# Optimization experiments

Hardware: AMD Instinct MI355X
Metric: run time of the kernel (lower is better)

Reference implementation:

```python
import jax, jax.numpy as jnp
import numpy as np

# init config (must satisfy k1+...+k6 == N_HEAD; k1==0 makes the source's
# off-by-k1 slice indices in get_sinusoid coincide with the correct ones)
K1, K2, K3, K4, K5, K6 = 0, 2, 2, 2, 1, 1
N_HEAD = K1 + K2 + K3 + K4 + K5 + K6  # 8
DILATIONS = (2.0, 4.0, 8.0, 16.0)     # length k4+k5+k6
TRUNC = 200.0                          # hard-coded T[T > 200] = 0 threshold


def setup_inputs() -> dict:
    key = jax.random.key(0)
    k_eta, k_nu, k_theta = jax.random.split(key, 3)
    return {
        "eta": jax.random.uniform(k_eta, (1, 1, 1), dtype=jnp.float32),  # >0 so tanh(eta)>0
        "nu": jax.random.normal(k_nu, (1, 1, 1), dtype=jnp.float32),
        "theta": jax.random.normal(k_theta, (1, 1, 1), dtype=jnp.float32),
        "query_len": 2048,
        "key_len": 2048,
    }


def reference(eta, nu, theta, query_len, key_len):
    k1, k2, k3, k4, k5, k6 = K1, K2, K3, K4, K5, K6
    undil_n = k1 + k2 + k3

    # --- Toeplitz |i-j| matrix, truncated: entries > 200 zeroed ---
    i = jnp.arange(query_len, dtype=jnp.float32)[:, None]
    j = jnp.arange(key_len, dtype=jnp.float32)[None, :]
    T = jnp.abs(i - j)                       # (Lq, Lk)
    T = jnp.where(T > TRUNC, 0.0, T)

    # --- dilated heads: L/d where L % d == 0 else 0 (vectorized over heads) ---
    d = jnp.asarray(DILATIONS, dtype=jnp.float32)[:, None, None]  # (dil_n,1,1)
    ind = (jnp.mod(T[None], d) == 0).astype(jnp.float32)
    Ld = (T[None] / d) * ind                 # (dil_n, Lq, Lk)

    Lu = jnp.broadcast_to(T[None], (undil_n, query_len, key_len))
    L = jnp.concatenate([Lu, Ld], axis=0)    # (n_head, Lq, Lk)

    lambda_ = jnp.tanh(eta)
    gamma = jax.nn.sigmoid(nu)

    # --- sinusoids (slice indices replicate the source exactly; k1=0) ---
    M = L * theta
    s2 = jnp.cos(M[k1:k1 + k2])
    s3 = jnp.sin(M[k2:k2 + k3])
    s5 = jnp.cos(M[k2 + k3 + k4:k2 + k3 + k4 + k5])
    s6 = jnp.sin(M[k2 + k3 + k4 + k5:])

    L1 = L[:k1]
    L2 = L[k1:k1 + k2]
    L3 = L[k1 + k2:k1 + k2 + k3]
    L4 = L[k1 + k2 + k3:k1 + k2 + k3 + k4]
    L5 = L[k1 + k2 + k3 + k4:k1 + k2 + k3 + k4 + k5]
    L6 = L[k1 + k2 + k3 + k4 + k5:]

    P1 = jnp.power(lambda_, L1)
    P4 = jnp.power(lambda_, L4)
    P2 = jnp.power(gamma, L2) * s2
    P3 = jnp.power(gamma, L3) * s3
    P5 = jnp.power(gamma, L5) * s5
    P6 = jnp.power(gamma, L6) * s6

    REM = jnp.concatenate([P1, P2, P3, P4, P5, P6], axis=0)  # (n_head, Lq, Lk)
    return jnp.transpose(REM, (1, 2, 0))                      # (Lq, Lk, n_head)
```

## Files before the change

kernel.cpp:

```cpp
#include <hip/hip_runtime.h>


#define EXP2F(x) __builtin_amdgcn_exp2f(x)
#define LOG2F(x) __builtin_amdgcn_logf(x)
#define SIN_RAD(x) __builtin_amdgcn_sinf((x) * 0.15915494309189535f)
#define COS_RAD(x) __builtin_amdgcn_cosf((x) * 0.15915494309189535f)

__global__ __launch_bounds__(256) void rem_kernel(
    const float* __restrict__ eta_p,
    const float* __restrict__ nu_p,
    const float* __restrict__ theta_p,
    const int*   __restrict__ klen_p,
    float* __restrict__ out,
    int total)
{
    int idx = blockIdx.x * 256 + threadIdx.x;
    if (idx >= total) return;

    int kl = klen_p[0];
    int i  = idx / kl;
    int j  = idx - i * kl;
    int d  = i - j;
    int Ti = d < 0 ? -d : d;
    if (Ti > 200) Ti = 0;

    float eta   = eta_p[0];
    float nu    = nu_p[0];
    float theta = theta_p[0];
    float e2e = EXP2F(2.0f * eta * 1.4426950408889634f);
    float lam = (e2e - 1.0f) / (e2e + 1.0f);
    float gam = 1.0f / (1.0f + EXP2F(-nu * 1.4426950408889634f));
    float l2l = LOG2F(lam);
    float l2g = LOG2F(gam);

    float Tf = (float)Ti;
    float c = COS_RAD(theta * Tf);
    float s = SIN_RAD(theta * Tf);
    float gT = EXP2F(Tf * l2g);
    float v01 = gT * c;
    float v23 = gT * s;

    float L2f  = (Ti & 1)  ? 0.0f : (float)(Ti >> 1);
    float L4f  = (Ti & 3)  ? 0.0f : (float)(Ti >> 2);
    float L8f  = (Ti & 7)  ? 0.0f : (float)(Ti >> 3);
    float L16f = (Ti & 15) ? 0.0f : (float)(Ti >> 4);

    float v4 = EXP2F(L2f * l2l);
    float v5 = EXP2F(L4f * l2l);
    float v6 = EXP2F(L8f  * l2g) * COS_RAD(theta * L8f);
    float v7 = EXP2F(L16f * l2g) * SIN_RAD(theta * L16f);

    float4* o = (float4*)(out + (size_t)idx * 8);
    o[0] = make_float4(v01, v01, v23, v23);
    o[1] = make_float4(v4, v5, v6, v7);
}

extern "C" void kernel_launch(void* const* d_in, const int* in_sizes, int n_in,
                              void* d_out, int out_size, void* d_ws, size_t ws_size,
                              hipStream_t stream) {
    const float* eta   = (const float*)d_in[0];
    const float* nu    = (const float*)d_in[1];
    const float* theta = (const float*)d_in[2];
    const int* klen = (const int*)d_in[4];

    int total = out_size / 8;
    int blocks = (total + 255) / 256;
    rem_kernel<<<blocks, 256, 0, stream>>>(eta, nu, theta, klen,
                                           (float*)d_out, total);
}
```

Baseline: 143.0 us.

## Split per-pair work across threads, fast-path truncated zeros, precompute scalars

```diff
diff --git a/kernel.cpp b/kernel.cpp
--- a/kernel.cpp
+++ b/kernel.cpp
@@ -3,56 +3,68 @@
 
 #define EXP2F(x) __builtin_amdgcn_exp2f(x)
 #define LOG2F(x) __builtin_amdgcn_logf(x)
-#define SIN_RAD(x) __builtin_amdgcn_sinf((x) * 0.15915494309189535f)
-#define COS_RAD(x) __builtin_amdgcn_cosf((x) * 0.15915494309189535f)
+#define SINR(x)  __builtin_amdgcn_sinf(x)
+#define COSR(x)  __builtin_amdgcn_cosf(x)
+#define INV2PI 0.15915494309189535f
+#define LOG2E  1.4426950408889634f
 
-__global__ __launch_bounds__(256) void rem_kernel(
-    const float* __restrict__ eta_p,
-    const float* __restrict__ nu_p,
-    const float* __restrict__ theta_p,
+__global__ void rem_setup(const float* __restrict__ eta,
+                          const float* __restrict__ nu,
+                          const float* __restrict__ theta,
+                          float* __restrict__ ws)
+{
+    if (threadIdx.x == 0 && blockIdx.x == 0) {
+        float e2e = EXP2F(2.0f * eta[0] * LOG2E);
+        float lam = (e2e - 1.0f) / (e2e + 1.0f);
+        float gam = 1.0f / (1.0f + EXP2F(-nu[0] * LOG2E));
+        ws[0] = LOG2F(lam);
+        ws[1] = LOG2F(gam);
+        ws[2] = theta[0] * INV2PI;
+    }
+}
+
+__global__ __launch_bounds__(256) void rem_main(
+    const float* __restrict__ ws,
     const int*   __restrict__ klen_p,
     float* __restrict__ out,
-    int total)
+    int nquads)
 {
-    int idx = blockIdx.x * 256 + threadIdx.x;
-    if (idx >= total) return;
+    int q = blockIdx.x * 256 + threadIdx.x;
+    if (q >= nquads) return;
 
-    int kl = klen_p[0];
-    int i  = idx / kl;
-    int j  = idx - i * kl;
-    int d  = i - j;
-    int Ti = d < 0 ? -d : d;
+    int kl   = klen_p[0];
+    int pair = q >> 1;
+    int sel  = q & 1;
+    int i    = pair / kl;
+    int j    = pair - i * kl;
+    int d    = i - j;
+    int Ti   = d < 0 ? -d : d;
     if (Ti > 200) Ti = 0;
 
-    float eta   = eta_p[0];
-    float nu    = nu_p[0];
-    float theta = theta_p[0];
-    float e2e = EXP2F(2.0f * eta * 1.4426950408889634f);
-    float lam = (e2e - 1.0f) / (e2e + 1.0f);
-    float gam = 1.0f / (1.0f + EXP2F(-nu * 1.4426950408889634f));
-    float l2l = LOG2F(lam);
-    float l2g = LOG2F(gam);
-
-    float Tf = (float)Ti;
-    float c = COS_RAD(theta * Tf);
-    float s = SIN_RAD(theta * Tf);
-    float gT = EXP2F(Tf * l2g);
-    float v01 = gT * c;
-    float v23 = gT * s;
-
-    float L2f  = (Ti & 1)  ? 0.0f : (float)(Ti >> 1);
-    float L4f  = (Ti & 3)  ? 0.0f : (float)(Ti >> 2);
-    float L8f  = (Ti & 7)  ? 0.0f : (float)(Ti >> 3);
-    float L16f = (Ti & 15) ? 0.0f : (float)(Ti >> 4);
-
-    float v4 = EXP2F(L2f * l2l);
-    float v5 = EXP2F(L4f * l2l);
-    float v6 = EXP2F(L8f  * l2g) * COS_RAD(theta * L8f);
-    float v7 = EXP2F(L16f * l2g) * SIN_RAD(theta * L16f);
-
-    float4* o = (float4*)(out + (size_t)idx * 8);
-    o[0] = make_float4(v01, v01, v23, v23);
-    o[1] = make_float4(v4, v5, v6, v7);
+    float4 v;
+    if (Ti == 0) {
+        v = sel ? make_float4(1.0f, 1.0f, 1.0f, 0.0f)
+                : make_float4(1.0f, 1.0f, 0.0f, 0.0f);
+    } else {
+        float l2l = ws[0], l2g = ws[1], thr = ws[2];
+        float Tf = (float)Ti;
+        if (sel == 0) {
+            float c  = COSR(thr * Tf);
+            float s  = SINR(thr * Tf);
+            float gT = EXP2F(Tf * l2g);
+            v = make_float4(gT * c, gT * c, gT * s, gT * s);
+        } else {
+            float L2f  = (Ti & 1)  ? 0.0f : (float)(Ti >> 1);
+            float L4f  = (Ti & 3)  ? 0.0f : (float)(Ti >> 2);
+            float L8f  = (Ti & 7)  ? 0.0f : (float)(Ti >> 3);
+            float L16f = (Ti & 15) ? 0.0f : (float)(Ti >> 4);
+            v = make_float4(EXP2F(L2f  * l2l),
+                            EXP2F(L4f  * l2l),
+                            EXP2F(L8f  * l2g) * COSR(thr * L8f),
+                            EXP2F(L16f * l2g) * SINR(thr * L16f));
+        }
+    }
+    ((float4*)out)[q] = v;
 }
 
 extern "C" void kernel_launch(void* const* d_in, const int* in_sizes, int n_in,
@@ -61,10 +73,12 @@
     const float* eta   = (const float*)d_in[0];
     const float* nu    = (const float*)d_in[1];
     const float* theta = (const float*)d_in[2];
-    const int* klen = (const int*)d_in[4];
+    const int*   klen  = (const int*)d_in[4];
+    float* ws = (float*)d_ws;
 
-    int total = out_size / 8;
-    int blocks = (total + 255) / 256;
-    rem_kernel<<<blocks, 256, 0, stream>>>(eta, nu, theta, klen,
-                                           (float*)d_out, total);
+    rem_setup<<<1, 64, 0, stream>>>(eta, nu, theta, ws);
+
+    int nquads = out_size / 4;
+    int blocks = (nquads + 255) / 256;
+    rem_main<<<blocks, 256, 0, stream>>>(ws, klen, (float*)d_out, nquads);
 }
```

Result: no change. 140.7 us (-1.6%).
